# Performance work log

Measured on AMD Instinct MI355X. Metric: run time of the kernel, lower is better.

## Reference

```python
import jax, jax.numpy as jnp
import numpy as np

B, T, CIN = 8, 4096, 512
GROUP, ENTRY = 2, 320
COUT = 512
D = COUT // GROUP  # per-group codebook dim = 256


def setup_inputs() -> dict:
    key = jax.random.key(0)
    k_x, k_w, k_cb, k_g = jax.random.split(key, 4)
    x = jax.random.normal(k_x, (B, T, CIN), dtype=jnp.float32)
    # weight_proj: Linear(in_channel, group*entry)
    Wp = jax.random.normal(k_w, (GROUP * ENTRY, CIN), dtype=jnp.float32) * (1.0 / np.sqrt(CIN))
    bp = jnp.zeros((GROUP * ENTRY,), dtype=jnp.float32)
    # stacked codebooks: [group, entry, out_channel//group]
    codebooks = jax.random.normal(k_cb, (GROUP, ENTRY, D), dtype=jnp.float32)
    # pre-sampled gumbel noise (torch gumbel_softmax samples this internally)
    gumbel = jax.random.gumbel(k_g, (B, T, GROUP * ENTRY), dtype=jnp.float32)
    return {"x": x, "Wp": Wp, "bp": bp, "codebooks": codebooks, "gumbel": gumbel}


def reference(x, Wp, bp, codebooks, gumbel):
    # weight_proj
    logits = jnp.einsum('btc,ec->bte', x, Wp) + bp          # [B,T,group*entry]
    # gumbel_softmax(tau=1, hard=False, dim=-1): softmax over full group*entry axis
    y = jax.nn.softmax(logits + gumbel, axis=-1)            # [B,T,group*entry]
    # chunk into groups -> contiguous reshape matches torch.chunk
    yg = y.reshape(B, T, GROUP, ENTRY)                      # [B,T,G,E]
    # per-group matmul against codebook weights, then concat over groups
    out = jnp.einsum('btge,ged->btgd', yg, codebooks)       # [B,T,G,D]
    return out.reshape(B, T, GROUP * D)                     # [B,T,out_channel]
```

## Files before the change

kernel.cpp:

```cpp
#include <hip/hip_runtime.h>
#include <stdint.h>

#define BT     32768
#define CIN    512
#define NE     640
#define ENTRY  320
#define DD     256
#define MROWS  64
#define TPB    512

using bf16x8 = __attribute__((ext_vector_type(8))) short;
using f32x4  = __attribute__((ext_vector_type(4))) float;

#define S_OFF      81920
#define SMEM_BYTES 82176

__device__ __forceinline__ unsigned short f2b(float f) {
    union { float f; uint32_t u; } v; v.f = f;
    uint32_t u = v.u;
    return (unsigned short)((u + 0x7FFFu + ((u >> 16) & 1u)) >> 16);
}

__global__ void prep_kernel(const float* __restrict__ Wp, const float* __restrict__ cb,
                            unsigned short* __restrict__ WpB2, unsigned short* __restrict__ cbT2) {
    int i = blockIdx.x * blockDim.x + threadIdx.x;
    if (i < NE * CIN) {
        int ks  = i / 20480;
        int rem = i - ks * 20480;
        int e   = rem >> 5;
        int kk  = rem & 31;
        WpB2[i] = f2b(Wp[e * CIN + ks * 32 + kk]);
    } else {
        int o = i - NE * CIN;
        if (o < 2 * ENTRY * DD) {
            int kk = o & 31;
            int t  = o >> 5;
            int n  = t & 255;
            int t2 = t >> 8;
            int ks = t2 % 10;
            int g  = t2 / 10;
            cbT2[o] = f2b(cb[(g * ENTRY + ks * 32 + kk) * DD + n]);
        }
    }
}

#define MFMA16(d, a, b) d = __builtin_amdgcn_mfma_f32_16x16x32_bf16(a, b, d, 0, 0, 0)

__global__ __launch_bounds__(TPB, 2) void fused_kernel(
    const float* __restrict__ x, const float* __restrict__ bp,
    const float* __restrict__ gum, const unsigned short* __restrict__ WpB2,
    const unsigned short* __restrict__ cbT2, float* __restrict__ out) {

    extern __shared__ char smem[];
    float* sS = (float*)(smem + S_OFF);

    const int tid = threadIdx.x;
    const int w  = tid >> 6;
    const int l  = tid & 63;
    const int q  = l >> 4;
    const int ln = l & 15;
    const int wr = w >> 2;
    const int wc = w & 3;
    const int rowbase = blockIdx.x * MROWS;
    const int swz = (ln & 7) << 4;

    if (tid < MROWS) sS[tid] = 0.0f;

    {
        const int ar  = tid >> 3;
        const int akq = tid & 7;
        const float* xrow = x + (size_t)(rowbase + ar) * CIN + akq * 4;
        const int abase = ar * 1024;
        const int aswz  = (ar & 7) << 4;
#pragma unroll
        for (int c = 0; c < 16; ++c) {
            float4 xv = *(const float4*)(xrow + c * 32);
            ushort4 hv;
            hv.x = f2b(xv.x); hv.y = f2b(xv.y); hv.z = f2b(xv.z); hv.w = f2b(xv.w);
            *(ushort4*)(smem + abase + ((c * 64 + akq * 8) ^ aswz)) = hv;
        }
    }
    __syncthreads();

    f32x4 acc1[2][10];
    const f32x4 fz = {0.f, 0.f, 0.f, 0.f};
#pragma unroll
    for (int rt = 0; rt < 2; ++rt)
#pragma unroll
        for (int ct = 0; ct < 10; ++ct) acc1[rt][ct] = fz;

    const int blane = ln * 32 + q * 8;
    const unsigned short* bptr = WpB2 + (wc * 160) * 32 + blane;
    const int aB = (wr * 32 + ln) * 1024;

    bf16x8 pA[10], pB[10];
    bf16x8 aA0, aA1, aB0, aB1;
#pragma unroll
    for (int ct = 0; ct < 10; ++ct) pA[ct] = *(const bf16x8*)(bptr + ct * 512);
    {
        const int at = (q * 16) ^ swz;
        aA0 = *(const bf16x8*)(smem + aB + at);
        aA1 = *(const bf16x8*)(smem + aB + 16384 + at);
    }

#pragma unroll 1
    for (int ks2 = 0; ks2 < 16; ks2 += 2) {
        {
            const unsigned short* pk = bptr + (ks2 + 1) * 20480;
#pragma unroll
            for (int ct = 0; ct < 10; ++ct) pB[ct] = *(const bf16x8*)(pk + ct * 512);
            const int at = ((ks2 + 1) * 64 + q * 16) ^ swz;
            aB0 = *(const bf16x8*)(smem + aB + at);
            aB1 = *(const bf16x8*)(smem + aB + 16384 + at);
        }
#pragma unroll
        for (int ct = 0; ct < 10; ++ct) {
            MFMA16(acc1[0][ct], aA0, pA[ct]);
            MFMA16(acc1[1][ct], aA1, pA[ct]);
        }
        if (ks2 + 2 < 16) {
            const unsigned short* pk = bptr + (ks2 + 2) * 20480;
#pragma unroll
            for (int ct = 0; ct < 10; ++ct) pA[ct] = *(const bf16x8*)(pk + ct * 512);
            const int at = ((ks2 + 2) * 64 + q * 16) ^ swz;
            aA0 = *(const bf16x8*)(smem + aB + at);
            aA1 = *(const bf16x8*)(smem + aB + 16384 + at);
        }
#pragma unroll
        for (int ct = 0; ct < 10; ++ct) {
            MFMA16(acc1[0][ct], aB0, pB[ct]);
            MFMA16(acc1[1][ct], aB1, pB[ct]);
        }
    }
    __syncthreads();

    const int g  = wc >> 1;
    const int nb = (wc & 1) * 128;
    const unsigned short* cptr = cbT2 + (size_t)g * 81920 + nb * 32 + blane;
    bf16x8 cA[8], cB[8];
#pragma unroll
    for (int ct = 0; ct < 8; ++ct) cA[ct] = *(const bf16x8*)(cptr + ct * 512);

    float bpv[10];
#pragma unroll
    for (int ct = 0; ct < 10; ++ct) bpv[ct] = bp[wc * 160 + ct * 16 + ln];

#pragma unroll
    for (int ri = 0; ri < 8; ++ri) {
        int rt = ri >> 2, r = ri & 3;
        int lrow = wr * 32 + rt * 16 + q * 4 + r;
        const float* pg = gum + (size_t)(rowbase + lrow) * NE + wc * 160 + ln;
        int ybase = lrow * 1280;
        int yswz  = (lrow & 7) << 4;
        float p = 0.f;
#pragma unroll
        for (int ct = 0; ct < 10; ++ct) {
            int col = wc * 160 + ct * 16 + ln;
            float v = acc1[rt][ct][r] + bpv[ct] + pg[ct * 16];
            float e = __expf(v);
            *(unsigned short*)(smem + ybase + ((col * 2) ^ yswz)) = f2b(e);
            p += e;
        }
        p += __shfl_xor(p, 1);
        p += __shfl_xor(p, 2);
        p += __shfl_xor(p, 4);
        p += __shfl_xor(p, 8);
        if (ln == 0) atomicAdd(&sS[lrow], p);
    }
    __syncthreads();

    f32x4 acc2[2][8];
#pragma unroll
    for (int rt = 0; rt < 2; ++rt)
#pragma unroll
        for (int ct = 0; ct < 8; ++ct) acc2[rt][ct] = fz;

    const int yB = (wr * 32 + ln) * 1280;
    bf16x8 yA0, yA1, yB0, yB1;
    {
        const int at = (g * 640 + q * 16) ^ swz;
        yA0 = *(const bf16x8*)(smem + yB + at);
        yA1 = *(const bf16x8*)(smem + yB + 20480 + at);
    }

#pragma unroll 1
    for (int ks2 = 0; ks2 < 10; ks2 += 2) {
        {
            const unsigned short* pk = cptr + (ks2 + 1) * 8192;
#pragma unroll
            for (int ct = 0; ct < 8; ++ct) cB[ct] = *(const bf16x8*)(pk + ct * 512);
            const int at = (g * 640 + (ks2 + 1) * 64 + q * 16) ^ swz;
            yB0 = *(const bf16x8*)(smem + yB + at);
            yB1 = *(const bf16x8*)(smem + yB + 20480 + at);
        }
#pragma unroll
        for (int ct = 0; ct < 8; ++ct) {
            MFMA16(acc2[0][ct], yA0, cA[ct]);
            MFMA16(acc2[1][ct], yA1, cA[ct]);
        }
        if (ks2 + 2 < 10) {
            const unsigned short* pk = cptr + (ks2 + 2) * 8192;
#pragma unroll
            for (int ct = 0; ct < 8; ++ct) cA[ct] = *(const bf16x8*)(pk + ct * 512);
            const int at = (g * 640 + (ks2 + 2) * 64 + q * 16) ^ swz;
            yA0 = *(const bf16x8*)(smem + yB + at);
            yA1 = *(const bf16x8*)(smem + yB + 20480 + at);
        }
#pragma unroll
        for (int ct = 0; ct < 8; ++ct) {
            MFMA16(acc2[0][ct], yB0, cB[ct]);
            MFMA16(acc2[1][ct], yB1, cB[ct]);
        }
    }

#pragma unroll
    for (int rt = 0; rt < 2; ++rt) {
#pragma unroll
        for (int r = 0; r < 4; ++r) {
            int lrow = wr * 32 + rt * 16 + q * 4 + r;
            float inv = 1.0f / sS[lrow];
            size_t orow = (size_t)(rowbase + lrow) * 512;
#pragma unroll
            for (int ct = 0; ct < 8; ++ct) {
                int col = g * 256 + nb + ct * 16 + ln;
                out[orow + col] = acc2[rt][ct][r] * inv;
            }
        }
    }
}

extern "C" void kernel_launch(void* const* d_in, const int* in_sizes, int n_in,
                              void* d_out, int out_size, void* d_ws, size_t ws_size,
                              hipStream_t stream) {
    const float* x   = (const float*)d_in[0];
    const float* Wp  = (const float*)d_in[1];
    const float* bp  = (const float*)d_in[2];
    const float* cb  = (const float*)d_in[3];
    const float* gum = (const float*)d_in[4];
    float* out = (float*)d_out;

    unsigned short* WpB2 = (unsigned short*)d_ws;
    unsigned short* cbT2 = WpB2 + NE * CIN;

    int prep_total = NE * CIN + 2 * ENTRY * DD;
    prep_kernel<<<(prep_total + 255) / 256, 256, 0, stream>>>(Wp, cb, WpB2, cbT2);

    fused_kernel<<<dim3(BT / MROWS), dim3(TPB), SMEM_BYTES, stream>>>(x, bp, gum, WpB2, cbT2, out);
}
```

Measured before the change: 250.7 us.

## Halve block tile, stream x directly into MFMA fragments, drop shared-memory staging

The block shrinks to 32 rows and 256 threads. Each wave now computes 80 logit columns in two halves, which cuts accumulator registers so three blocks can share a CU. The x tile is no longer staged in shared memory: it is read from global memory, converted to bf16 inside the pipelined K loop, and used directly as MFMA A-fragments. Shared-memory atomics for the row sums are replaced by per-wave partial sums that are added at the end. The risk is that the Wp and codebook fragments are now reused over only half as many rows, so global and L2 weight traffic per output roughly doubles.

```diff
diff --git a/kernel.cpp b/kernel.cpp
--- a/kernel.cpp
+++ b/kernel.cpp
@@ -6,19 +6,28 @@
 #define NE     640
 #define ENTRY  320
 #define DD     256
-#define MROWS  64
-#define TPB    512
+#define MROWS  32
+#define TPB    256
 
 using bf16x8 = __attribute__((ext_vector_type(8))) short;
 using f32x4  = __attribute__((ext_vector_type(4))) float;
 
-#define S_OFF      81920
-#define SMEM_BYTES 82176
+#define PS_OFF     40960
+#define SMEM_BYTES 41472
 
 __device__ __forceinline__ unsigned short f2b(float f) {
     union { float f; uint32_t u; } v; v.f = f;
     uint32_t u = v.u;
     return (unsigned short)((u + 0x7FFFu + ((u >> 16) & 1u)) >> 16);
+}
+
+__device__ __forceinline__ bf16x8 cvt8(float4 a, float4 b) {
+    bf16x8 t;
+    t[0] = (short)f2b(a.x); t[1] = (short)f2b(a.y);
+    t[2] = (short)f2b(a.z); t[3] = (short)f2b(a.w);
+    t[4] = (short)f2b(b.x); t[5] = (short)f2b(b.y);
+    t[6] = (short)f2b(b.z); t[7] = (short)f2b(b.w);
+    return t;
 }
 
 __global__ void prep_kernel(const float* __restrict__ Wp, const float* __restrict__ cb,
@@ -46,127 +55,135 @@
 
 #define MFMA16(d, a, b) d = __builtin_amdgcn_mfma_f32_16x16x32_bf16(a, b, d, 0, 0, 0)
 
-__global__ __launch_bounds__(TPB, 2) void fused_kernel(
+__global__ __launch_bounds__(TPB, 3) void fused_kernel(
     const float* __restrict__ x, const float* __restrict__ bp,
     const float* __restrict__ gum, const unsigned short* __restrict__ WpB2,
     const unsigned short* __restrict__ cbT2, float* __restrict__ out) {
 
     extern __shared__ char smem[];
-    float* sS = (float*)(smem + S_OFF);
+    float* pS = (float*)(smem + PS_OFF);
 
     const int tid = threadIdx.x;
     const int w  = tid >> 6;
     const int l  = tid & 63;
     const int q  = l >> 4;
     const int ln = l & 15;
-    const int wr = w >> 2;
-    const int wc = w & 3;
     const int rowbase = blockIdx.x * MROWS;
     const int swz = (ln & 7) << 4;
-
-    if (tid < MROWS) sS[tid] = 0.0f;
-
-    {
-        const int ar  = tid >> 3;
-        const int akq = tid & 7;
-        const float* xrow = x + (size_t)(rowbase + ar) * CIN + akq * 4;
-        const int abase = ar * 1024;
-        const int aswz  = (ar & 7) << 4;
-#pragma unroll
-        for (int c = 0; c < 16; ++c) {
-            float4 xv = *(const float4*)(xrow + c * 32);
-            ushort4 hv;
-            hv.x = f2b(xv.x); hv.y = f2b(xv.y); hv.z = f2b(xv.z); hv.w = f2b(xv.w);
-            *(ushort4*)(smem + abase + ((c * 64 + akq * 8) ^ aswz)) = hv;
-        }
-    }
-    __syncthreads();
-
-    f32x4 acc1[2][10];
+    const int blane = ln * 32 + q * 8;
+
+    const float* xbase = x + (size_t)(rowbase + ln) * CIN + q * 8;
+
+    float pr[8];
+#pragma unroll
+    for (int i = 0; i < 8; ++i) pr[i] = 0.f;
+
     const f32x4 fz = {0.f, 0.f, 0.f, 0.f};
-#pragma unroll
-    for (int rt = 0; rt < 2; ++rt)
-#pragma unroll
-        for (int ct = 0; ct < 10; ++ct) acc1[rt][ct] = fz;
-
-    const int blane = ln * 32 + q * 8;
-    const unsigned short* bptr = WpB2 + (wc * 160) * 32 + blane;
-    const int aB = (wr * 32 + ln) * 1024;
-
-    bf16x8 pA[10], pB[10];
-    bf16x8 aA0, aA1, aB0, aB1;
-#pragma unroll
-    for (int ct = 0; ct < 10; ++ct) pA[ct] = *(const bf16x8*)(bptr + ct * 512);
-    {
-        const int at = (q * 16) ^ swz;
-        aA0 = *(const bf16x8*)(smem + aB + at);
-        aA1 = *(const bf16x8*)(smem + aB + 16384 + at);
-    }
 
 #pragma unroll 1
-    for (int ks2 = 0; ks2 < 16; ks2 += 2) {
+    for (int h = 0; h < 2; ++h) {
+        const unsigned short* bh = WpB2 + (h * 320 + w * 80) * 32 + blane;
+
+        f32x4 acc[2][5];
+#pragma unroll
+        for (int rt = 0; rt < 2; ++rt)
+#pragma unroll
+            for (int ct = 0; ct < 5; ++ct) acc[rt][ct] = fz;
+
+        bf16x8 pA[5], pB[5];
+        bf16x8 afA0, afA1, afB0, afB1;
         {
-            const unsigned short* pk = bptr + (ks2 + 1) * 20480;
-#pragma unroll
-            for (int ct = 0; ct < 10; ++ct) pB[ct] = *(const bf16x8*)(pk + ct * 512);
-            const int at = ((ks2 + 1) * 64 + q * 16) ^ swz;
-            aB0 = *(const bf16x8*)(smem + aB + at);
-            aB1 = *(const bf16x8*)(smem + aB + 16384 + at);
-        }
-#pragma unroll
-        for (int ct = 0; ct < 10; ++ct) {
-            MFMA16(acc1[0][ct], aA0, pA[ct]);
-            MFMA16(acc1[1][ct], aA1, pA[ct]);
-        }
-        if (ks2 + 2 < 16) {
-            const unsigned short* pk = bptr + (ks2 + 2) * 20480;
-#pragma unroll
-            for (int ct = 0; ct < 10; ++ct) pA[ct] = *(const bf16x8*)(pk + ct * 512);
-            const int at = ((ks2 + 2) * 64 + q * 16) ^ swz;
-            aA0 = *(const bf16x8*)(smem + aB + at);
-            aA1 = *(const bf16x8*)(smem + aB + 16384 + at);
-        }
-#pragma unroll
-        for (int ct = 0; ct < 10; ++ct) {
-            MFMA16(acc1[0][ct], aB0, pB[ct]);
-            MFMA16(acc1[1][ct], aB1, pB[ct]);
-        }
-    }
-    __syncthreads();
-
-    const int g  = wc >> 1;
-    const int nb = (wc & 1) * 128;
+            float4 r0 = *(const float4*)(xbase);
+            float4 r1 = *(const float4*)(xbase + 4);
+            float4 r2 = *(const float4*)(xbase + 16 * CIN);
+            float4 r3 = *(const float4*)(xbase + 16 * CIN + 4);
+#pragma unroll
+            for (int ct = 0; ct < 5; ++ct) pA[ct] = *(const bf16x8*)(bh + ct * 512);
+            afA0 = cvt8(r0, r1); afA1 = cvt8(r2, r3);
+        }
+
+#pragma unroll 1
+        for (int ks2 = 0; ks2 < 16; ks2 += 2) {
+            {
+                const unsigned short* pk = bh + (ks2 + 1) * 20480;
+                const float* xp = xbase + (ks2 + 1) * 32;
+                float4 r0 = *(const float4*)(xp);
+                float4 r1 = *(const float4*)(xp + 4);
+                float4 r2 = *(const float4*)(xp + 16 * CIN);
+                float4 r3 = *(const float4*)(xp + 16 * CIN + 4);
+#pragma unroll
+                for (int ct = 0; ct < 5; ++ct) pB[ct] = *(const bf16x8*)(pk + ct * 512);
+#pragma unroll
+                for (int ct = 0; ct < 5; ++ct) {
+                    MFMA16(acc[0][ct], afA0, pA[ct]);
+                    MFMA16(acc[1][ct], afA1, pA[ct]);
+                }
+                afB0 = cvt8(r0, r1); afB1 = cvt8(r2, r3);
+            }
+            {
+                float4 r0, r1, r2, r3;
+                if (ks2 + 2 < 16) {
+                    const unsigned short* pk = bh + (ks2 + 2) * 20480;
+                    const float* xp = xbase + (ks2 + 2) * 32;
+                    r0 = *(const float4*)(xp);
+                    r1 = *(const float4*)(xp + 4);
+                    r2 = *(const float4*)(xp + 16 * CIN);
+                    r3 = *(const float4*)(xp + 16 * CIN + 4);
+#pragma unroll
+                    for (int ct = 0; ct < 5; ++ct) pA[ct] = *(const bf16x8*)(pk + ct * 512);
+                }
+#pragma unroll
+                for (int ct = 0; ct < 5; ++ct) {
+                    MFMA16(acc[0][ct], afB0, pB[ct]);
+                    MFMA16(acc[1][ct], afB1, pB[ct]);
+                }
+                if (ks2 + 2 < 16) { afA0 = cvt8(r0, r1); afA1 = cvt8(r2, r3); }
+            }
+        }
+
+        float bpv[5];
+#pragma unroll
+        for (int ct = 0; ct < 5; ++ct) bpv[ct] = bp[h * 320 + w * 80 + ct * 16 + ln];
+
+#pragma unroll
+        for (int ri = 0; ri < 8; ++ri) {
+            int rt = ri >> 2, r = ri & 3;
+            int row = rt * 16 + q * 4 + r;
+            const float* pg = gum + (size_t)(rowbase + row) * NE + h * 320 + w * 80 + ln;
+            int ybase = row * 1280;
+            int yswz  = (row & 7) << 4;
+            float p = 0.f;
+#pragma unroll
+            for (int ct = 0; ct < 5; ++ct) {
+                int colb = (h * 320 + w * 80 + ct * 16 + ln) * 2;
+                float v = acc[rt][ct][r] + bpv[ct] + pg[ct * 16];
+                float e = __expf(v);
+                *(unsigned short*)(smem + ybase + (colb ^ yswz)) = f2b(e);
+                p += e;
+            }
+            p += __shfl_xor(p, 1);
+            p += __shfl_xor(p, 2);
+            p += __shfl_xor(p, 4);
+            p += __shfl_xor(p, 8);
+            pr[ri] += p;
+        }
+    }
+
+    if (ln == 0) {
+#pragma unroll
+        for (int ri = 0; ri < 8; ++ri) {
+            int row = (ri >> 2) * 16 + q * 4 + (ri & 3);
+            pS[row * 4 + w] = pr[ri];
+        }
+    }
+
+    const int g  = w >> 1;
+    const int nb = (w & 1) * 128;
     const unsigned short* cptr = cbT2 + (size_t)g * 81920 + nb * 32 + blane;
     bf16x8 cA[8], cB[8];
 #pragma unroll
     for (int ct = 0; ct < 8; ++ct) cA[ct] = *(const bf16x8*)(cptr + ct * 512);
 
-    float bpv[10];
-#pragma unroll
-    for (int ct = 0; ct < 10; ++ct) bpv[ct] = bp[wc * 160 + ct * 16 + ln];
-
-#pragma unroll
-    for (int ri = 0; ri < 8; ++ri) {
-        int rt = ri >> 2, r = ri & 3;
-        int lrow = wr * 32 + rt * 16 + q * 4 + r;
-        const float* pg = gum + (size_t)(rowbase + lrow) * NE + wc * 160 + ln;
-        int ybase = lrow * 1280;
-        int yswz  = (lrow & 7) << 4;
-        float p = 0.f;
-#pragma unroll
-        for (int ct = 0; ct < 10; ++ct) {
-            int col = wc * 160 + ct * 16 + ln;
-            float v = acc1[rt][ct][r] + bpv[ct] + pg[ct * 16];
-            float e = __expf(v);
-            *(unsigned short*)(smem + ybase + ((col * 2) ^ yswz)) = f2b(e);
-            p += e;
-        }
-        p += __shfl_xor(p, 1);
-        p += __shfl_xor(p, 2);
-        p += __shfl_xor(p, 4);
-        p += __shfl_xor(p, 8);
-        if (ln == 0) atomicAdd(&sS[lrow], p);
-    }
     __syncthreads();
 
     f32x4 acc2[2][8];
@@ -175,7 +192,7 @@
 #pragma unroll
         for (int ct = 0; ct < 8; ++ct) acc2[rt][ct] = fz;
 
-    const int yB = (wr * 32 + ln) * 1280;
+    const int yB = ln * 1280;
     bf16x8 yA0, yA1, yB0, yB1;
     {
         const int at = (g * 640 + q * 16) ^ swz;
@@ -217,9 +234,10 @@
     for (int rt = 0; rt < 2; ++rt) {
 #pragma unroll
         for (int r = 0; r < 4; ++r) {
-            int lrow = wr * 32 + rt * 16 + q * 4 + r;
-            float inv = 1.0f / sS[lrow];
-            size_t orow = (size_t)(rowbase + lrow) * 512;
+            int row = rt * 16 + q * 4 + r;
+            float4 sv = *(const float4*)(pS + row * 4);
+            float inv = 1.0f / (sv.x + sv.y + sv.z + sv.w);
+            size_t orow = (size_t)(rowbase + row) * 512;
 #pragma unroll
             for (int ct = 0; ct < 8; ++ct) {
                 int col = g * 256 + nb + ct * 16 + ln;
```

Result: slower. 356.2 us (+42.0%).
